# Optimization experiments

Measured on AMD Instinct MI355X. Metric: run time of the kernel, lower is better.

The kernel has to match this reference:

```python
import jax, jax.numpy as jnp
import numpy as np

# Izhikevich parameters (regular spiking defaults)
A = 0.02     # recovery time scale
B = 0.2      # sensitivity of recovery
C = -65.0    # reset voltage
D = 8.0      # recovery reset increment
VTH = 30.0   # spike threshold
BETA = 1.0   # surrogate gradient sharpness
DT = 0.5     # integration time step (ms)


@jax.custom_vjp
def spike_fn(v):
    # Heaviside forward, surrogate sigmoid-derivative backward
    return (v >= VTH).astype(v.dtype)

def _spike_fwd(v):
    return spike_fn(v), v

def _spike_bwd(v, g):
    s = jax.nn.sigmoid(BETA * (v - VTH))
    return (g * (BETA * s * (1.0 - s)),)

spike_fn.defvjp(_spike_fwd, _spike_bwd)


def setup_inputs() -> dict:
    key = jax.random.key(0)
    input_current = jax.random.normal(key, (32, 2000, 512), dtype=jnp.float32)
    return {"input_current": input_current}


def reference(input_current):
    # input_current: [batch, n_steps, n_neurons]
    batch, n_steps, n_neurons = input_current.shape
    dtype = input_current.dtype
    v0 = jnp.full((batch, n_neurons), C, dtype=dtype)
    u0 = jnp.full((batch, n_neurons), B * C, dtype=dtype)

    def step(carry, i_t):
        v, u = carry
        dv = (0.04 * v * v + 5.0 * v + 140.0 - u + i_t) * DT
        du = A * (B * v - u) * DT
        v = v + dv
        u = u + du
        s = spike_fn(v)
        v = v * (1.0 - s) + C * s
        u = u + D * s
        return (v, u), (s, v, u)

    xs = jnp.swapaxes(input_current, 0, 1)  # [n_steps, batch, n_neurons]
    _, (spikes, voltages, recovery) = jax.lax.scan(step, (v0, u0), xs)
    # back to [batch, n_steps, n_neurons]
    spikes = jnp.swapaxes(spikes, 0, 1)
    voltages = jnp.swapaxes(voltages, 0, 1)
    recovery = jnp.swapaxes(recovery, 0, 1)
    return spikes, voltages, recovery
```

## Files before the change

### kernel.cpp

```cpp
#include <hip/hip_runtime.h>


#define NSTEPS 2000
#define NNEUR  512
#define BATCH  32
#define INPLANE 1024000u
#define PLANE  32768000u
#define CHUNK  100
#define NCHUNK (NSTEPS / CHUNK)
#define NG     (CHUNK / 4)

typedef const __attribute__((address_space(1))) unsigned GPtr;
typedef __attribute__((address_space(3))) unsigned LPtr;

__device__ __forceinline__ void izh_step(float i_t, float& v, float& u, float& s) {
#pragma clang fp contract(off)
    float t1 = 0.04f * v;
    t1 = t1 * v;
    float t2 = 5.0f * v;
    float acc = t1 + t2;
    acc = acc + 140.0f;
    acc = acc - u;
    acc = acc + i_t;
    float dv = acc * 0.5f;
    float t4 = 0.2f * v;
    t4 = t4 - u;
    t4 = 0.02f * t4;
    float du = t4 * 0.5f;
    v = v + dv;
    u = u + du;
    bool sp = (v >= 30.0f);
    s = sp ? 1.0f : 0.0f;
    v = sp ? -65.0f : v;
    u = sp ? (u + 8.0f) : u;
}

template <int W>
__device__ __forceinline__ void run_compute(const float (*lin)[CHUNK * 64], int lane,
                                            unsigned voff, float* __restrict__ out) {
    float* oplane = out + (size_t)W * PLANE;
    float v = -65.0f;
    float u = -13.0f;

    asm volatile("s_barrier" ::: "memory");
    for (int c = 0; c < NCHUNK; ++c) {
        const float* lbuf = &lin[c & 1][0];
        float ra[4], rb[4];
#pragma unroll
        for (int j = 0; j < 4; ++j) ra[j] = lbuf[j * 64 + lane];

        for (int g = 0; g < NG - 1; g += 2) {
#pragma unroll
            for (int j = 0; j < 4; ++j) rb[j] = lbuf[(4 * (g + 1) + j) * 64 + lane];
#pragma unroll
            for (int j = 0; j < 4; ++j) {
                float s;
                izh_step(ra[j], v, u, s);
                oplane[voff] = (W == 0) ? s : (W == 1) ? v : u;
                voff += NNEUR;
            }
            if (g + 2 < NG) {
#pragma unroll
                for (int j = 0; j < 4; ++j) ra[j] = lbuf[(4 * (g + 2) + j) * 64 + lane];
            }
#pragma unroll
            for (int j = 0; j < 4; ++j) {
                float s;
                izh_step(rb[j], v, u, s);
                oplane[voff] = (W == 0) ? s : (W == 1) ? v : u;
                voff += NNEUR;
            }
        }
#pragma unroll
        for (int j = 0; j < 4; ++j) {
            float s;
            izh_step(ra[j], v, u, s);
            oplane[voff] = (W == 0) ? s : (W == 1) ? v : u;
            voff += NNEUR;
        }
        asm volatile("s_barrier" ::: "memory");
    }
}

__global__ __launch_bounds__(256, 1) void izh_kernel(const float* __restrict__ in,
                                                     float* __restrict__ out) {
    __shared__ float lin[2][CHUNK * 64];

    const int tid  = threadIdx.x;
    const int w    = tid >> 6;
    const int lane = tid & 63;
    const unsigned n0 = (unsigned)((blockIdx.x * 64) & (NNEUR - 1));
    const unsigned b  = (unsigned)((unsigned)(blockIdx.x * 64) >> 9);

    if (w == 3) {
        const float* gsrc = in + (size_t)b * INPLANE
                               + (size_t)(lane >> 4) * NNEUR
                               + n0 + (size_t)(lane & 15) * 4;
#pragma unroll
        for (int g = 0; g < NG; ++g) {
            __builtin_amdgcn_global_load_lds((GPtr*)(gsrc + (size_t)(4 * g) * NNEUR),
                                             (LPtr*)&lin[0][g * 256], 16, 0, 0);
        }
        asm volatile("s_waitcnt vmcnt(0)" ::: "memory");
        asm volatile("s_barrier" ::: "memory");

        for (int c = 0; c < NCHUNK; ++c) {
            if (c + 1 < NCHUNK) {
                const float* gs = gsrc + (size_t)(c + 1) * CHUNK * NNEUR;
                float* lb = &lin[(c + 1) & 1][0];
#pragma unroll
                for (int g = 0; g < NG; ++g) {
                    __builtin_amdgcn_global_load_lds((GPtr*)(gs + (size_t)(4 * g) * NNEUR),
                                                     (LPtr*)(lb + g * 256), 16, 0, 0);
                }
                asm volatile("s_waitcnt vmcnt(0)" ::: "memory");
            }
            asm volatile("s_barrier" ::: "memory");
        }
    } else {
        const unsigned voff0 = b * INPLANE + n0 + (unsigned)lane;
        if (w == 0)      run_compute<0>(lin, lane, voff0, out);
        else if (w == 1) run_compute<1>(lin, lane, voff0, out);
        else             run_compute<2>(lin, lane, voff0, out);
    }
}

extern "C" void kernel_launch(void* const* d_in, const int* in_sizes, int n_in,
                              void* d_out, int out_size, void* d_ws, size_t ws_size,
                              hipStream_t stream) {
    const float* in = (const float*)d_in[0];
    float* out = (float*)d_out;
    izh_kernel<<<(BATCH * NNEUR) / 64, 256, 0, stream>>>(in, out);
}
```

Measured before the change: 493.0 us.

## Split scan into checkpoint pass and parallel segment replay pass

Replaces the single producer/consumer kernel with two kernels. The first runs the full recurrence per neuron without writing outputs, saving v/u checkpoints at each 100-step chunk boundary into workspace. The second launches one block per (chunk, neuron group), restarts from the checkpoint and writes spikes, voltages and recovery in parallel across chunks, which removes the serial write bottleneck and raises occupancy. In exchange the input is read twice and the recurrence is computed twice, and the serial first pass stays on the critical path.

```diff
diff --git a/kernel.cpp b/kernel.cpp
--- a/kernel.cpp
+++ b/kernel.cpp
@@ -9,6 +9,8 @@
 #define CHUNK  100
 #define NCHUNK (NSTEPS / CHUNK)
 #define NG     (CHUNK / 4)
+#define NCHAIN 16384u
+#define WIN    10
 
 typedef const __attribute__((address_space(1))) unsigned GPtr;
 typedef __attribute__((address_space(3))) unsigned LPtr;
@@ -35,93 +37,113 @@
     u = sp ? (u + 8.0f) : u;
 }
 
-template <int W>
-__device__ __forceinline__ void run_compute(const float (*lin)[CHUNK * 64], int lane,
-                                            unsigned voff, float* __restrict__ out) {
-    float* oplane = out + (size_t)W * PLANE;
-    float v = -65.0f;
-    float u = -13.0f;
+__global__ __launch_bounds__(64, 1) void izh_pass1(const float* __restrict__ in,
+                                                   float* __restrict__ ckV,
+                                                   float* __restrict__ ckU) {
+    __shared__ float lin[2][CHUNK * 64];
 
-    asm volatile("s_barrier" ::: "memory");
+    const int lane = threadIdx.x;
+    const unsigned gid = blockIdx.x * 64u + (unsigned)lane;
+    const unsigned b   = gid >> 9;
+    const unsigned n0  = (unsigned)((blockIdx.x * 64) & (NNEUR - 1));
+    const float* gsrc = in + (size_t)b * INPLANE + (size_t)(lane >> 4) * NNEUR
+                           + n0 + (size_t)(lane & 15) * 4;
+#pragma unroll
+    for (int g = 0; g < NG; ++g)
+        __builtin_amdgcn_global_load_lds((GPtr*)(gsrc + (size_t)(4 * g) * NNEUR),
+                                         (LPtr*)&lin[0][g * 256], 16, 0, 0);
+
+    float v = -65.0f, u = -13.0f;
     for (int c = 0; c < NCHUNK; ++c) {
+        asm volatile("s_waitcnt vmcnt(0)" ::: "memory");
+        if (c + 1 < NCHUNK) {
+            const float* gs = gsrc + (size_t)(c + 1) * CHUNK * NNEUR;
+            float* lb = &lin[(c + 1) & 1][0];
+#pragma unroll
+            for (int g = 0; g < NG; ++g)
+                __builtin_amdgcn_global_load_lds((GPtr*)(gs + (size_t)(4 * g) * NNEUR),
+                                                 (LPtr*)(lb + g * 256), 16, 0, 0);
+        }
+        {
+            float vc = v, uc = u;
+            ckV[(unsigned)c * NCHAIN + gid] = vc;
+            ckU[(unsigned)c * NCHAIN + gid] = uc;
+        }
         const float* lbuf = &lin[c & 1][0];
-        float ra[4], rb[4];
+        float ra[WIN], rb[WIN];
 #pragma unroll
-        for (int j = 0; j < 4; ++j) ra[j] = lbuf[j * 64 + lane];
-
-        for (int g = 0; g < NG - 1; g += 2) {
+        for (int j = 0; j < WIN; ++j) ra[j] = lbuf[j * 64 + lane];
+        for (int w = 0; w < CHUNK / WIN; w += 2) {
 #pragma unroll
-            for (int j = 0; j < 4; ++j) rb[j] = lbuf[(4 * (g + 1) + j) * 64 + lane];
+            for (int j = 0; j < WIN; ++j) rb[j] = lbuf[((w + 1) * WIN + j) * 64 + lane];
 #pragma unroll
-            for (int j = 0; j < 4; ++j) {
-                float s;
-                izh_step(ra[j], v, u, s);
-                oplane[voff] = (W == 0) ? s : (W == 1) ? v : u;
-                voff += NNEUR;
-            }
-            if (g + 2 < NG) {
+            for (int j = 0; j < WIN; ++j) { float s; izh_step(ra[j], v, u, s); }
+            if (w + 2 < CHUNK / WIN) {
 #pragma unroll
-                for (int j = 0; j < 4; ++j) ra[j] = lbuf[(4 * (g + 2) + j) * 64 + lane];
+                for (int j = 0; j < WIN; ++j) ra[j] = lbuf[((w + 2) * WIN + j) * 64 + lane];
             }
 #pragma unroll
-            for (int j = 0; j < 4; ++j) {
-                float s;
-                izh_step(rb[j], v, u, s);
-                oplane[voff] = (W == 0) ? s : (W == 1) ? v : u;
-                voff += NNEUR;
-            }
+            for (int j = 0; j < WIN; ++j) { float s; izh_step(rb[j], v, u, s); }
         }
-#pragma unroll
-        for (int j = 0; j < 4; ++j) {
-            float s;
-            izh_step(ra[j], v, u, s);
-            oplane[voff] = (W == 0) ? s : (W == 1) ? v : u;
-            voff += NNEUR;
-        }
-        asm volatile("s_barrier" ::: "memory");
     }
 }
 
-__global__ __launch_bounds__(256, 1) void izh_kernel(const float* __restrict__ in,
-                                                     float* __restrict__ out) {
-    __shared__ float lin[2][CHUNK * 64];
+__global__ __launch_bounds__(64, 4) void izh_pass2(const float* __restrict__ in,
+                                                   float* __restrict__ out,
+                                                   const float* __restrict__ ckV,
+                                                   const float* __restrict__ ckU) {
+    const int lane = threadIdx.x;
+    const unsigned sp  = (unsigned)blockIdx.x & 255u;
+    const unsigned seg = (unsigned)blockIdx.x >> 8;
+    const unsigned gid = sp * 64u + (unsigned)lane;
+    const unsigned b   = gid >> 9;
+    const unsigned n   = gid & (NNEUR - 1);
 
-    const int tid  = threadIdx.x;
-    const int w    = tid >> 6;
-    const int lane = tid & 63;
-    const unsigned n0 = (unsigned)((blockIdx.x * 64) & (NNEUR - 1));
-    const unsigned b  = (unsigned)((unsigned)(blockIdx.x * 64) >> 9);
+    float v = ckV[seg * NCHAIN + gid];
+    float u = ckU[seg * NCHAIN + gid];
 
-    if (w == 3) {
-        const float* gsrc = in + (size_t)b * INPLANE
-                               + (size_t)(lane >> 4) * NNEUR
-                               + n0 + (size_t)(lane & 15) * 4;
+    const size_t base = (size_t)b * INPLANE + (size_t)seg * CHUNK * NNEUR + n;
+    const float* ip = in + base;
+    float* oS = out;
+    float* oV = out + (size_t)PLANE;
+    float* oU = out + 2 * (size_t)PLANE;
+    size_t off = base;
+
+    float ra[WIN], rb[WIN];
 #pragma unroll
-        for (int g = 0; g < NG; ++g) {
-            __builtin_amdgcn_global_load_lds((GPtr*)(gsrc + (size_t)(4 * g) * NNEUR),
-                                             (LPtr*)&lin[0][g * 256], 16, 0, 0);
+    for (int j = 0; j < WIN; ++j) ra[j] = ip[(size_t)j * NNEUR];
+
+    for (int w = 0; w < CHUNK / WIN; w += 2) {
+#pragma unroll
+        for (int j = 0; j < WIN; ++j) rb[j] = ip[(size_t)((w + 1) * WIN + j) * NNEUR];
+        {
+            float sB[WIN], vB[WIN], uB[WIN];
+#pragma unroll
+            for (int j = 0; j < WIN; ++j) { izh_step(ra[j], v, u, sB[j]); vB[j] = v; uB[j] = u; }
+#pragma unroll
+            for (int j = 0; j < WIN; ++j) {
+                oS[off + (size_t)j * NNEUR] = sB[j];
+                oV[off + (size_t)j * NNEUR] = vB[j];
+                oU[off + (size_t)j * NNEUR] = uB[j];
+            }
+            off += (size_t)WIN * NNEUR;
         }
-        asm volatile("s_waitcnt vmcnt(0)" ::: "memory");
-        asm volatile("s_barrier" ::: "memory");
-
-        for (int c = 0; c < NCHUNK; ++c) {
-            if (c + 1 < NCHUNK) {
-                const float* gs = gsrc + (size_t)(c + 1) * CHUNK * NNEUR;
-                float* lb = &lin[(c + 1) & 1][0];
+        if (w + 2 < CHUNK / WIN) {
 #pragma unroll
-                for (int g = 0; g < NG; ++g) {
-                    __builtin_amdgcn_global_load_lds((GPtr*)(gs + (size_t)(4 * g) * NNEUR),
-                                                     (LPtr*)(lb + g * 256), 16, 0, 0);
-                }
-                asm volatile("s_waitcnt vmcnt(0)" ::: "memory");
+            for (int j = 0; j < WIN; ++j) ra[j] = ip[(size_t)((w + 2) * WIN + j) * NNEUR];
+        }
+        {
+            float sB[WIN], vB[WIN], uB[WIN];
+#pragma unroll
+            for (int j = 0; j < WIN; ++j) { izh_step(rb[j], v, u, sB[j]); vB[j] = v; uB[j] = u; }
+#pragma unroll
+            for (int j = 0; j < WIN; ++j) {
+                oS[off + (size_t)j * NNEUR] = sB[j];
+                oV[off + (size_t)j * NNEUR] = vB[j];
+                oU[off + (size_t)j * NNEUR] = uB[j];
             }
-            asm volatile("s_barrier" ::: "memory");
+            off += (size_t)WIN * NNEUR;
         }
-    } else {
-        const unsigned voff0 = b * INPLANE + n0 + (unsigned)lane;
-        if (w == 0)      run_compute<0>(lin, lane, voff0, out);
-        else if (w == 1) run_compute<1>(lin, lane, voff0, out);
-        else             run_compute<2>(lin, lane, voff0, out);
     }
 }
 
@@ -130,5 +152,8 @@
                               hipStream_t stream) {
     const float* in = (const float*)d_in[0];
     float* out = (float*)d_out;
-    izh_kernel<<<(BATCH * NNEUR) / 64, 256, 0, stream>>>(in, out);
+    float* ckV = (float*)d_ws;
+    float* ckU = ckV + (size_t)NCHUNK * NCHAIN;
+    izh_pass1<<<256, 64, 0, stream>>>(in, ckV, ckU);
+    izh_pass2<<<NCHUNK * 256, 64, 0, stream>>>(in, out, ckV, ckU);
 }
```

Measured after the change: 538.2 us. 9.2% more time.
